# Optimization experiments

Hardware: AMD Instinct MI355X
Metric: run time of the kernel (lower is better)

The kernel has to match this reference:

```python
import jax, jax.numpy as jnp
import numpy as np

EMBED_DIM = 1024
HEAD_NUM = 16
NEG = 100000.0


def setup_inputs() -> dict:
    key = jax.random.key(0)
    k1, k2, k3, k4, k5 = jax.random.split(key, 5)
    B, S, E = 2, 2048, EMBED_DIM
    return {
        "x": jax.random.normal(k1, (B, S, E), dtype=jnp.float32),
        "w_attn": jax.random.normal(k2, (E, 3 * E), dtype=jnp.float32) * 0.02,
        "b_attn": jax.random.normal(k3, (3 * E,), dtype=jnp.float32) * 0.02,
        "w_proj": jax.random.normal(k4, (E, E), dtype=jnp.float32) * 0.02,
        "b_proj": jax.random.normal(k5, (E,), dtype=jnp.float32) * 0.02,
    }


def reference(x, w_attn, b_attn, w_proj, b_proj):
    B, S, E = x.shape
    H = HEAD_NUM
    d = E // H
    dk = jnp.asarray(d, x.dtype) ** 0.5  # (embed_dim // head_num) ** 0.5

    qkv = x @ w_attn + b_attn                      # [B, S, 3E]
    qkv = qkv.reshape(B, S, H, 3 * d)              # split heads BEFORE chunk (as in source)
    qkv = jnp.swapaxes(qkv, 1, 2)                  # [B, H, S, 3d]
    q, k, v = jnp.split(qkv, 3, axis=-1)           # each [B, H, S, d]

    w = jnp.einsum("bhqd,bhkd->bhqk", q, k) / dk   # [B, H, S, S]
    mask = jnp.tril(jnp.ones((S, S), dtype=x.dtype))
    w = w * mask - (1.0 - mask) * NEG              # exact masking math of source
    w = jax.nn.softmax(w, axis=-1)                 # dropout omitted (eval mode)

    a = jnp.einsum("bhqk,bhkd->bhqd", w, v)        # [B, H, S, d]
    a = jnp.swapaxes(a, 1, 2).reshape(B, S, E)     # [B, S, E]
    h = a @ w_proj + b_proj                        # resi dropout omitted (eval mode)
    return h
```

## Files before the change

### kernel.cpp

```cpp
#include <hip/hip_runtime.h>
#include <hip/hip_bf16.h>

#define BB 2
#define SS 2048
#define EE 1024
#define HH 16
#define DD 64
#define MM (BB*SS)
#define N1 (3*EE)

typedef __attribute__((ext_vector_type(4))) float f32x4;
typedef __attribute__((ext_vector_type(16))) float f32x16;
typedef __attribute__((ext_vector_type(8))) short bf16x8;
typedef __attribute__((ext_vector_type(4))) unsigned int u32x4;
typedef __attribute__((ext_vector_type(2))) unsigned int u32x2;

__device__ __forceinline__ ushort f2bf(float f){
  union { float f; unsigned u; } v; v.f = f;
  unsigned r = v.u + 0x7fffu + ((v.u >> 16) & 1u);
  return (ushort)(r >> 16);
}

__device__ __forceinline__ float bf2f(ushort u){
  union { unsigned u; float f; } v; v.u = ((unsigned)u) << 16; return v.f;
}

__device__ __forceinline__ unsigned cvt_pk(float a, float b){
  unsigned r; asm("v_cvt_pk_bf16_f32 %0, %1, %2" : "=v"(r) : "v"(a), "v"(b)); return r;
}

__device__ __forceinline__ float exp2_fast(float x){
  float r; asm("v_exp_f32 %0, %1" : "=v"(r) : "v"(x)); return r;
}

__device__ __forceinline__ u32x2 pl32swap(unsigned a, unsigned b){
  return __builtin_amdgcn_permlane32_swap(a, b, false, false);
}

__device__ __forceinline__ void gload16(const void* g, void* l){
  __builtin_amdgcn_global_load_lds(
      (const __attribute__((address_space(1))) unsigned*)g,
      (__attribute__((address_space(3))) unsigned*)l, 16, 0, 0);
}

__global__ __launch_bounds__(256) void prep_kernel(const float* __restrict__ x, ushort* __restrict__ xb,
    const float* __restrict__ wa, ushort* __restrict__ waT,
    const float* __restrict__ wp, ushort* __restrict__ wpT){
  __shared__ float t[32][33];
  const int bid = blockIdx.x, tid = threadIdx.x;
  if (bid < 4096){
    int i = bid*256 + tid;
    const float4 f = reinterpret_cast<const float4*>(x)[i];
    ushort4 o; o.x=f2bf(f.x); o.y=f2bf(f.y); o.z=f2bf(f.z); o.w=f2bf(f.w);
    reinterpret_cast<ushort4*>(xb)[i] = o;
  } else {
    const float* in; ushort* out; int N, nx, b;
    if (bid < 7168){ b = bid - 4096; in = wa; out = waT; N = N1; nx = N1/32; }
    else           { b = bid - 7168; in = wp; out = wpT; N = EE; nx = EE/32; }
    const int n0 = (b % nx)*32, k0 = (b / nx)*32;
    const int tx = tid & 31, ty = tid >> 5;
    for (int r = ty; r < 32; r += 8)
      t[r][tx] = in[(size_t)(k0+r)*N + n0 + tx];
    __syncthreads();
    for (int r = ty; r < 32; r += 8)
      out[(size_t)(n0+r)*EE + k0 + tx] = f2bf(t[tx][r]);
  }
}

__global__ __launch_bounds__(512) void gemm_qkv(const ushort* __restrict__ A,
    const ushort* __restrict__ Bt, const float* __restrict__ bias,
    ushort* __restrict__ q_, ushort* __restrict__ k_, ushort* __restrict__ v_,
    int M, int N, int K){
  __shared__ ushort As[256*64];
  __shared__ ushort Bs[128*64];
  const int tid = threadIdx.x;
  const int lane = tid & 63, w = tid >> 6;
  const int nx = gridDim.x;
  const int nwg = nx * gridDim.y;
  const int flat = blockIdx.y*nx + blockIdx.x;
  const int sw = (flat & 7)*(nwg >> 3) + (flat >> 3);
  const int m0 = (sw / nx)*256, n0 = (sw % nx)*128;
  const int wm = (w >> 1)*64, wn = (w & 1)*64;
  const int lr = lane & 15, g4 = lane >> 4;
  const int csr = lane >> 3;
  const int gcb = ((lane & 7) ^ csr)*8;
  const int sw7 = lr & 7;

  f32x4 acc[4][4] = {};
  for (int k0 = 0; k0 < K; k0 += 64){
    #pragma unroll
    for (int i = 0; i < 4; ++i){
      const int c = w*4 + i;
      gload16(A + (size_t)(m0 + c*8 + csr)*K + k0 + gcb, &As[(c*8)*64]);
    }
    #pragma unroll
    for (int i = 0; i < 2; ++i){
      const int c = w*2 + i;
      gload16(Bt + (size_t)(n0 + c*8 + csr)*K + k0 + gcb, &Bs[(c*8)*64]);
    }
    __syncthreads();
    #pragma unroll
    for (int kk = 0; kk < 2; ++kk){
      bf16x8 af[4], bfr[4];
      #pragma unroll
      for (int m = 0; m < 4; ++m)
        af[m] = *reinterpret_cast<bf16x8*>(&As[(wm + m*16 + lr)*64 + (((kk*4 + g4) ^ sw7)*8)]);
      #pragma unroll
      for (int n = 0; n < 4; ++n)
        bfr[n] = *reinterpret_cast<bf16x8*>(&Bs[(wn + n*16 + lr)*64 + (((kk*4 + g4) ^ sw7)*8)]);
      __builtin_amdgcn_s_setprio(1);
      #pragma unroll
      for (int m = 0; m < 4; ++m)
        #pragma unroll
        for (int n = 0; n < 4; ++n)
          acc[m][n] = __builtin_amdgcn_mfma_f32_16x16x32_bf16(af[m], bfr[n], acc[m][n], 0, 0, 0);
      __builtin_amdgcn_s_setprio(0);
    }
    __syncthreads();
  }
  #pragma unroll
  for (int m = 0; m < 4; ++m){
    #pragma unroll
    for (int n = 0; n < 4; ++n){
      int col = n0 + wn + n*16 + lr;
      float bv = bias[col];
      #pragma unroll
      for (int r = 0; r < 4; ++r){
        int row = m0 + wm + m*16 + (lane >> 4)*4 + r;
        float v = acc[m][n][r] + bv;
        int b = row >> 11, s = row & 2047;
        int h = col / 192, t = col - h*192;
        ushort u = f2bf(v);
        size_t bh = (size_t)(b*HH + h);
        if (t < 64)       q_[(bh*SS + s)*DD + t]        = u;
        else if (t < 128) k_[(bh*SS + s)*DD + (t-64)]   = u;
        else              v_[(bh*DD + (t-128))*SS + s]  = u;
      }
    }
  }
}

__global__ __launch_bounds__(256) void gemm_proj(const ushort* __restrict__ A,
    const ushort* __restrict__ Bt, const float* __restrict__ bias,
    float* __restrict__ of, int M, int N, int K){
  __shared__ ushort As[128*64];
  __shared__ ushort Bs[128*64];
  const int tid = threadIdx.x;
  const int lane = tid & 63, w = tid >> 6;
  const int nx = gridDim.x;
  const int nwg = nx * gridDim.y;
  const int flat = blockIdx.y*nx + blockIdx.x;
  const int sw = (flat & 7)*(nwg >> 3) + (flat >> 3);
  const int m0 = (sw / nx)*128, n0 = (sw % nx)*128;
  const int wm = (w >> 1)*64, wn = (w & 1)*64;
  const int lr = lane & 15, g4 = lane >> 4;
  const int c0 = w*4;
  const int csr = lane >> 3;
  const int gcb = ((lane & 7) ^ csr)*8;
  const int sw7 = lr & 7;

  f32x4 acc[4][4] = {};
  for (int k0 = 0; k0 < K; k0 += 64){
    #pragma unroll
    for (int i = 0; i < 4; ++i){
      const int c = c0 + i;
      gload16(A  + (size_t)(m0 + c*8 + csr)*K + k0 + gcb, &As[(c*8)*64]);
      gload16(Bt + (size_t)(n0 + c*8 + csr)*K + k0 + gcb, &Bs[(c*8)*64]);
    }
    __syncthreads();
    #pragma unroll
    for (int kk = 0; kk < 2; ++kk){
      bf16x8 af[4], bfr[4];
      #pragma unroll
      for (int m = 0; m < 4; ++m)
        af[m] = *reinterpret_cast<bf16x8*>(&As[(wm + m*16 + lr)*64 + (((kk*4 + g4) ^ sw7)*8)]);
      #pragma unroll
      for (int n = 0; n < 4; ++n)
        bfr[n] = *reinterpret_cast<bf16x8*>(&Bs[(wn + n*16 + lr)*64 + (((kk*4 + g4) ^ sw7)*8)]);
      __builtin_amdgcn_s_setprio(1);
      #pragma unroll
      for (int m = 0; m < 4; ++m)
        #pragma unroll
        for (int n = 0; n < 4; ++n)
          acc[m][n] = __builtin_amdgcn_mfma_f32_16x16x32_bf16(af[m], bfr[n], acc[m][n], 0, 0, 0);
      __builtin_amdgcn_s_setprio(0);
    }
    __syncthreads();
  }
  #pragma unroll
  for (int m = 0; m < 4; ++m){
    #pragma unroll
    for (int n = 0; n < 4; ++n){
      int col = n0 + wn + n*16 + lr;
      float bv = bias[col];
      #pragma unroll
      for (int r = 0; r < 4; ++r){
        int row = m0 + wm + m*16 + (lane >> 4)*4 + r;
        of[(size_t)row*N + col] = acc[m][n][r] + bv;
      }
    }
  }
}

#define SCL 0.18033688f
__global__ __launch_bounds__(256,3) void attn2(const ushort* __restrict__ Qg,
    const ushort* __restrict__ Kg, const ushort* __restrict__ Vg,
    ushort* __restrict__ aout, ushort* __restrict__ pbuf,
    float* __restrict__ s0b, float* __restrict__ s1b){
  __shared__ __align__(16) ushort Kl[3][64*64];
  __shared__ __align__(16) ushort Vl[3][64*64];
  const int tid = threadIdx.x, lane = tid & 63, wv = tid >> 6;
  const int bh = blockIdx.x;
  const int c  = blockIdx.y;
  int qt, t0, t1, half;
  if (c < 8){ qt = c; t0 = 0; t1 = 2*(c+1); half = -1; }
  else { int i = c - 8; qt = 8 + (i >> 1); int n = qt + 1; half = i & 1;
         t0 = half ? n : 0; t1 = half ? 2*n : n; }
  const int b = bh >> 4, h = bh & 15;
  const int q0 = qt*128;
  const int ql = lane & 31, g = lane >> 5;
  const int qrow = q0 + wv*32 + ql;
  const int qminw = q0 + wv*32;
  const int qmaxw = qminw + 31;

  const ushort* Qp = Qg + ((size_t)bh*SS + qrow)*DD;
  bf16x8 qf[4];
  #pragma unroll
  for (int s = 0; s < 4; ++s)
    qf[s] = *(const bf16x8*)(Qp + s*16 + g*8);

  f32x16 ot[2] = {};
  float sr = 0.f;

  const int csr = lane >> 3;
  const int gcb = ((lane & 7) ^ csr)*8;
  const ushort* Kbase = Kg + (size_t)bh*SS*DD;
  const ushort* Vbase = Vg + (size_t)bh*DD*SS;
  const int nv = (qmaxw >> 6) + 1;
  const int swq = (ql & 7);

  auto stage = [&](int t, int bi){
    const int k0 = t*64;
    #pragma unroll
    for (int i = 0; i < 2; ++i){
      const int ch = wv*2 + i;
      gload16(Kbase + (size_t)(k0 + ch*8 + csr)*DD + gcb, &Kl[bi][(ch*8)*64]);
      gload16(Vbase + (size_t)(ch*8 + csr)*SS + k0 + gcb, &Vl[bi][(ch*8)*64]);
    }
  };

  auto qk = [&](int t, int bi, f32x16& s0, f32x16& s1){
    const ushort* Kc = &Kl[bi][0];
    f32x16 a0 = {}, a1 = {};
    __builtin_amdgcn_s_setprio(1);
    #pragma unroll
    for (int s = 0; s < 4; ++s){
      bf16x8 kf0 = *(const bf16x8*)&Kc[ ql     *64 + (((2*s + g) ^ swq)*8)];
      bf16x8 kf1 = *(const bf16x8*)&Kc[(32+ql) *64 + (((2*s + g) ^ swq)*8)];
      a0 = __builtin_amdgcn_mfma_f32_32x32x16_bf16(kf0, qf[s], a0, 0, 0, 0);
      a1 = __builtin_amdgcn_mfma_f32_32x32x16_bf16(kf1, qf[s], a1, 0, 0, 0);
    }
    __builtin_amdgcn_s_setprio(0);
    const int k0 = t*64;
    if (k0 + 63 > qminw){
      #pragma unroll
      for (int r = 0; r < 16; ++r){
        int kg0 = k0 + (r & 3) + 8*(r >> 2) + 4*g;
        a0[r] = (kg0 > qrow) ? -1e30f : a0[r];
        a1[r] = (kg0 + 32 > qrow) ? -1e30f : a1[r];
      }
    }
    s0 = a0; s1 = a1;
  };

  auto smpv = [&](int bi, f32x16& s0, f32x16& s1){
    float p[2][16];
    #pragma unroll
    for (int r = 0; r < 16; ++r){
      p[0][r] = exp2_fast(s0[r]*SCL);
      p[1][r] = exp2_fast(s1[r]*SCL);
    }
    float s8[8];
    #pragma unroll
    for (int i = 0; i < 8; ++i)
      s8[i] = (p[0][i] + p[0][i+8]) + (p[1][i] + p[1][i+8]);
    float ts = ((s8[0]+s8[1]) + (s8[2]+s8[3])) + ((s8[4]+s8[5]) + (s8[6]+s8[7]));
    { u32x2 rs = pl32swap(__float_as_uint(ts), __float_as_uint(ts));
      ts = __uint_as_float(rs[0]) + __uint_as_float(rs[1]); }
    sr += ts;

    const ushort* Vc = &Vl[bi][0];
    __builtin_amdgcn_s_setprio(1);
    #pragma unroll
    for (int kf = 0; kf < 2; ++kf){
      #pragma unroll
      for (int s2 = 0; s2 < 2; ++s2){
        const int base = s2*8;
        unsigned u0 = cvt_pk(p[kf][base+0], p[kf][base+1]);
        unsigned u1 = cvt_pk(p[kf][base+2], p[kf][base+3]);
        unsigned u2 = cvt_pk(p[kf][base+4], p[kf][base+5]);
        unsigned u3 = cvt_pk(p[kf][base+6], p[kf][base+7]);
        u32x2 r0 = pl32swap(u0, u2);
        u32x2 r1 = pl32swap(u1, u3);
        union { u32x4 u; bf16x8 hv; } pw;
        pw.u[0] = r0[0]; pw.u[1] = r1[0]; pw.u[2] = r0[1]; pw.u[3] = r1[1];
        const int cbv = 4*kf + 2*s2 + g;
        bf16x8 v0f = *(const bf16x8*)&Vc[ ql     *64 + ((cbv ^ swq)*8)];
        bf16x8 v1f = *(const bf16x8*)&Vc[(32+ql) *64 + ((cbv ^ swq)*8)];
        ot[0] = __builtin_amdgcn_mfma_f32_32x32x16_bf16(v0f, pw.hv, ot[0], 0, 0, 0);
        ot[1] = __builtin_amdgcn_mfma_f32_32x32x16_bf16(v1f, pw.hv, ot[1], 0, 0, 0);
      }
    }
    __builtin_amdgcn_s_setprio(0);
  };

  stage(t0, 0);
  stage(t0 + 1, 1);
  int bi = 0;
  for (int t = t0; t < t1; ++t){
    if (t + 1 < t1) { asm volatile("s_waitcnt vmcnt(4)" ::: "memory"); }
    else            { asm volatile("s_waitcnt vmcnt(0)" ::: "memory"); }
    __builtin_amdgcn_s_barrier();
    __builtin_amdgcn_sched_barrier(0);
    if (t + 2 < t1){
      int bs = bi + 2; if (bs >= 3) bs -= 3;
      stage(t + 2, bs);
    }
    if (t < nv){
      f32x16 s0, s1;
      qk(t, bi, s0, s1);
      smpv(bi, s0, s1);
    }
    ++bi; if (bi == 3) bi = 0;
  }

  const float inv = 1.f / sr;
  if (half == 1){
    const int pr = ((qt - 8)*32 + bh)*128 + wv*32 + ql;
    #pragma unroll
    for (int df = 0; df < 2; ++df){
      #pragma unroll
      for (int t = 0; t < 4; ++t){
        ushort4 o4;
        o4.x = f2bf(ot[df][t*4+0]*inv);
        o4.y = f2bf(ot[df][t*4+1]*inv);
        o4.z = f2bf(ot[df][t*4+2]*inv);
        o4.w = f2bf(ot[df][t*4+3]*inv);
        int d = df*32 + 8*t + 4*g;
        *(ushort4*)&pbuf[(size_t)pr*64 + d] = o4;
      }
    }
    if (g == 0) s1b[pr] = sr;
  } else {
    const size_t obase = ((size_t)b*SS + qrow)*EE + h*DD;
    #pragma unroll
    for (int df = 0; df < 2; ++df){
      #pragma unroll
      for (int t = 0; t < 4; ++t){
        ushort4 o4;
        o4.x = f2bf(ot[df][t*4+0]*inv);
        o4.y = f2bf(ot[df][t*4+1]*inv);
        o4.z = f2bf(ot[df][t*4+2]*inv);
        o4.w = f2bf(ot[df][t*4+3]*inv);
        int d = df*32 + 8*t + 4*g;
        *(ushort4*)&aout[obase + d] = o4;
      }
    }
    if (half == 0){
      const int pr = ((qt - 8)*32 + bh)*128 + wv*32 + ql;
      if (g == 0) s0b[pr] = sr;
    }
  }
}

__global__ __launch_bounds__(256) void combine_kernel(ushort* __restrict__ ab,
    const ushort* __restrict__ pbuf, const float* __restrict__ s0b,
    const float* __restrict__ s1b){
  const int idx = blockIdx.x*256 + threadIdx.x;
  const int d4 = (idx & 15)*4;
  const int rr = (idx >> 4) & 127;
  const int pb = idx >> 11;
  const int qt8 = pb >> 5, bh = pb & 31;
  const int b = bh >> 4, h = bh & 15;
  const int pr = pb*128 + rr;
  const float s0 = s0b[pr], s1 = s1b[pr];
  const float wn = 1.f/(s0 + s1);
  const float w0 = s0*wn, w1 = s1*wn;
  const size_t ao = ((size_t)(b*SS + (8 + qt8)*128 + rr))*EE + h*DD + d4;
  const size_t po = (size_t)pr*64 + d4;
  ushort4 a = *(const ushort4*)&ab[ao];
  ushort4 p = *(const ushort4*)&pbuf[po];
  ushort4 o;
  o.x = f2bf(w0*bf2f(a.x) + w1*bf2f(p.x));
  o.y = f2bf(w0*bf2f(a.y) + w1*bf2f(p.y));
  o.z = f2bf(w0*bf2f(a.z) + w1*bf2f(p.z));
  o.w = f2bf(w0*bf2f(a.w) + w1*bf2f(p.w));
  *(ushort4*)&ab[ao] = o;
}

extern "C" void kernel_launch(void* const* d_in, const int* in_sizes, int n_in,
                              void* d_out, int out_size, void* d_ws, size_t ws_size,
                              hipStream_t stream){
  const float* x      = (const float*)d_in[0];
  const float* w_attn = (const float*)d_in[1];
  const float* b_attn = (const float*)d_in[2];
  const float* w_proj = (const float*)d_in[3];
  const float* b_proj = (const float*)d_in[4];
  float* out = (float*)d_out;

  ushort* ws   = (ushort*)d_ws;
  ushort* xb   = ws;
  ushort* waT  = xb  + (size_t)MM*EE;
  ushort* wpT  = waT + (size_t)N1*EE;
  ushort* qb_  = wpT + (size_t)EE*EE;
  ushort* kb_  = qb_ + (size_t)MM*EE;
  ushort* vTb  = kb_ + (size_t)MM*EE;
  ushort* ab   = vTb + (size_t)MM*EE;
  ushort* pbuf = xb;
  float*  s0b  = (float*)waT;
  float*  s1b  = s0b + 8*32*128;

  prep_kernel<<<8192, 256, 0, stream>>>(x, xb, w_attn, waT, w_proj, wpT);
  gemm_qkv<<<dim3(N1/128, MM/256), 512, 0, stream>>>(xb, waT, b_attn, qb_, kb_, vTb, MM, N1, EE);
  attn2<<<dim3(BB*HH, 24), 256, 0, stream>>>(qb_, kb_, vTb, ab, pbuf, s0b, s1b);
  combine_kernel<<<2048, 256, 0, stream>>>(ab, pbuf, s0b, s1b);
  gemm_proj<<<dim3(EE/128, MM/128), 256, 0, stream>>>(ab, wpT, b_proj, out, MM, EE, EE);
}
```

Baseline: 114.2 us.

## Split causal attention into up to four key-range parts and shrink GEMM tiles

The attention kernel now splits each query tile's key range into 1 to 4 parts depending on tile depth, launching 40 blocks per head instead of 24. Partial outputs and row sums go to a generalized buffer that the combine kernel merges. The K/V staging drops from triple to double buffering and occupancy is raised to 5 blocks per CU. Both GEMMs use smaller tiles to get more workgroups: 128x128 with 256 threads for QKV and 64x128 for the projection. The aim is better load balance and CU fill, at the cost of more combine traffic and less latency hiding in the attention loop.

```diff
diff --git a/kernel.cpp b/kernel.cpp
--- a/kernel.cpp
+++ b/kernel.cpp
@@ -42,6 +42,8 @@
       (const __attribute__((address_space(1))) unsigned*)g,
       (__attribute__((address_space(3))) unsigned*)l, 16, 0, 0);
 }
+
+__device__ __constant__ int exoff_c[16] = {0,0,0,0, 0,1,2,3, 4,6,8,10, 12,15,18,21};
 
 __global__ __launch_bounds__(256) void prep_kernel(const float* __restrict__ x, ushort* __restrict__ xb,
     const float* __restrict__ wa, ushort* __restrict__ waT,
@@ -67,82 +69,10 @@
   }
 }
 
-__global__ __launch_bounds__(512) void gemm_qkv(const ushort* __restrict__ A,
+__global__ __launch_bounds__(256) void gemm_qkv(const ushort* __restrict__ A,
     const ushort* __restrict__ Bt, const float* __restrict__ bias,
     ushort* __restrict__ q_, ushort* __restrict__ k_, ushort* __restrict__ v_,
     int M, int N, int K){
-  __shared__ ushort As[256*64];
-  __shared__ ushort Bs[128*64];
-  const int tid = threadIdx.x;
-  const int lane = tid & 63, w = tid >> 6;
-  const int nx = gridDim.x;
-  const int nwg = nx * gridDim.y;
-  const int flat = blockIdx.y*nx + blockIdx.x;
-  const int sw = (flat & 7)*(nwg >> 3) + (flat >> 3);
-  const int m0 = (sw / nx)*256, n0 = (sw % nx)*128;
-  const int wm = (w >> 1)*64, wn = (w & 1)*64;
-  const int lr = lane & 15, g4 = lane >> 4;
-  const int csr = lane >> 3;
-  const int gcb = ((lane & 7) ^ csr)*8;
-  const int sw7 = lr & 7;
-
-  f32x4 acc[4][4] = {};
-  for (int k0 = 0; k0 < K; k0 += 64){
-    #pragma unroll
-    for (int i = 0; i < 4; ++i){
-      const int c = w*4 + i;
-      gload16(A + (size_t)(m0 + c*8 + csr)*K + k0 + gcb, &As[(c*8)*64]);
-    }
-    #pragma unroll
-    for (int i = 0; i < 2; ++i){
-      const int c = w*2 + i;
-      gload16(Bt + (size_t)(n0 + c*8 + csr)*K + k0 + gcb, &Bs[(c*8)*64]);
-    }
-    __syncthreads();
-    #pragma unroll
-    for (int kk = 0; kk < 2; ++kk){
-      bf16x8 af[4], bfr[4];
-      #pragma unroll
-      for (int m = 0; m < 4; ++m)
-        af[m] = *reinterpret_cast<bf16x8*>(&As[(wm + m*16 + lr)*64 + (((kk*4 + g4) ^ sw7)*8)]);
-      #pragma unroll
-      for (int n = 0; n < 4; ++n)
-        bfr[n] = *reinterpret_cast<bf16x8*>(&Bs[(wn + n*16 + lr)*64 + (((kk*4 + g4) ^ sw7)*8)]);
-      __builtin_amdgcn_s_setprio(1);
-      #pragma unroll
-      for (int m = 0; m < 4; ++m)
-        #pragma unroll
-        for (int n = 0; n < 4; ++n)
-          acc[m][n] = __builtin_amdgcn_mfma_f32_16x16x32_bf16(af[m], bfr[n], acc[m][n], 0, 0, 0);
-      __builtin_amdgcn_s_setprio(0);
-    }
-    __syncthreads();
-  }
-  #pragma unroll
-  for (int m = 0; m < 4; ++m){
-    #pragma unroll
-    for (int n = 0; n < 4; ++n){
-      int col = n0 + wn + n*16 + lr;
-      float bv = bias[col];
-      #pragma unroll
-      for (int r = 0; r < 4; ++r){
-        int row = m0 + wm + m*16 + (lane >> 4)*4 + r;
-        float v = acc[m][n][r] + bv;
-        int b = row >> 11, s = row & 2047;
-        int h = col / 192, t = col - h*192;
-        ushort u = f2bf(v);
-        size_t bh = (size_t)(b*HH + h);
-        if (t < 64)       q_[(bh*SS + s)*DD + t]        = u;
-        else if (t < 128) k_[(bh*SS + s)*DD + (t-64)]   = u;
-        else              v_[(bh*DD + (t-128))*SS + s]  = u;
-      }
-    }
-  }
-}
-
-__global__ __launch_bounds__(256) void gemm_proj(const ushort* __restrict__ A,
-    const ushort* __restrict__ Bt, const float* __restrict__ bias,
-    float* __restrict__ of, int M, int N, int K){
   __shared__ ushort As[128*64];
   __shared__ ushort Bs[128*64];
   const int tid = threadIdx.x;
@@ -196,6 +126,77 @@
       #pragma unroll
       for (int r = 0; r < 4; ++r){
         int row = m0 + wm + m*16 + (lane >> 4)*4 + r;
+        float v = acc[m][n][r] + bv;
+        int b = row >> 11, s = row & 2047;
+        int h = col / 192, t = col - h*192;
+        ushort u = f2bf(v);
+        size_t bh = (size_t)(b*HH + h);
+        if (t < 64)       q_[(bh*SS + s)*DD + t]        = u;
+        else if (t < 128) k_[(bh*SS + s)*DD + (t-64)]   = u;
+        else              v_[(bh*DD + (t-128))*SS + s]  = u;
+      }
+    }
+  }
+}
+
+__global__ __launch_bounds__(256) void gemm_proj(const ushort* __restrict__ A,
+    const ushort* __restrict__ Bt, const float* __restrict__ bias,
+    float* __restrict__ of, int M, int N, int K){
+  __shared__ ushort As[64*64];
+  __shared__ ushort Bs[128*64];
+  const int tid = threadIdx.x;
+  const int lane = tid & 63, w = tid >> 6;
+  const int nx = gridDim.x;
+  const int nwg = nx * gridDim.y;
+  const int flat = blockIdx.y*nx + blockIdx.x;
+  const int sw = (flat & 7)*(nwg >> 3) + (flat >> 3);
+  const int m0 = (sw / nx)*64, n0 = (sw % nx)*128;
+  const int lr = lane & 15, g4 = lane >> 4;
+  const int csr = lane >> 3;
+  const int gcb = ((lane & 7) ^ csr)*8;
+  const int sw7 = lr & 7;
+
+  f32x4 acc[4][2] = {};
+  for (int k0 = 0; k0 < K; k0 += 64){
+    #pragma unroll
+    for (int i = 0; i < 2; ++i){
+      const int c = w*2 + i;
+      gload16(A + (size_t)(m0 + c*8 + csr)*K + k0 + gcb, &As[(c*8)*64]);
+    }
+    #pragma unroll
+    for (int i = 0; i < 4; ++i){
+      const int c = w*4 + i;
+      gload16(Bt + (size_t)(n0 + c*8 + csr)*K + k0 + gcb, &Bs[(c*8)*64]);
+    }
+    __syncthreads();
+    #pragma unroll
+    for (int kk = 0; kk < 2; ++kk){
+      bf16x8 af[4], bfr[2];
+      #pragma unroll
+      for (int m = 0; m < 4; ++m)
+        af[m] = *reinterpret_cast<bf16x8*>(&As[(m*16 + lr)*64 + (((kk*4 + g4) ^ sw7)*8)]);
+      #pragma unroll
+      for (int n = 0; n < 2; ++n)
+        bfr[n] = *reinterpret_cast<bf16x8*>(&Bs[(w*32 + n*16 + lr)*64 + (((kk*4 + g4) ^ sw7)*8)]);
+      __builtin_amdgcn_s_setprio(1);
+      #pragma unroll
+      for (int m = 0; m < 4; ++m)
+        #pragma unroll
+        for (int n = 0; n < 2; ++n)
+          acc[m][n] = __builtin_amdgcn_mfma_f32_16x16x32_bf16(af[m], bfr[n], acc[m][n], 0, 0, 0);
+      __builtin_amdgcn_s_setprio(0);
+    }
+    __syncthreads();
+  }
+  #pragma unroll
+  for (int m = 0; m < 4; ++m){
+    #pragma unroll
+    for (int n = 0; n < 2; ++n){
+      int col = n0 + w*32 + n*16 + lr;
+      float bv = bias[col];
+      #pragma unroll
+      for (int r = 0; r < 4; ++r){
+        int row = m0 + m*16 + g4*4 + r;
         of[(size_t)row*N + col] = acc[m][n][r] + bv;
       }
     }
@@ -203,19 +204,24 @@
 }
 
 #define SCL 0.18033688f
-__global__ __launch_bounds__(256,3) void attn2(const ushort* __restrict__ Qg,
+__global__ __launch_bounds__(256,5) void attn2(const ushort* __restrict__ Qg,
     const ushort* __restrict__ Kg, const ushort* __restrict__ Vg,
     ushort* __restrict__ aout, ushort* __restrict__ pbuf,
-    float* __restrict__ s0b, float* __restrict__ s1b){
-  __shared__ __align__(16) ushort Kl[3][64*64];
-  __shared__ __align__(16) ushort Vl[3][64*64];
+    float* __restrict__ sb){
+  __shared__ __align__(16) ushort Kl[2][64*64];
+  __shared__ __align__(16) ushort Vl[2][64*64];
   const int tid = threadIdx.x, lane = tid & 63, wv = tid >> 6;
   const int bh = blockIdx.x;
   const int c  = blockIdx.y;
-  int qt, t0, t1, half;
-  if (c < 8){ qt = c; t0 = 0; t1 = 2*(c+1); half = -1; }
-  else { int i = c - 8; qt = 8 + (i >> 1); int n = qt + 1; half = i & 1;
-         t0 = half ? n : 0; t1 = half ? 2*n : n; }
+  int qt, part;
+  if (c < 4)       { qt = c;                 part = 0; }
+  else if (c < 12) { qt = 4 + ((c-4) >> 1);  part = (c-4) & 1; }
+  else if (c < 24) { qt = 8 + (c-12)/3;      part = (c-12)%3; }
+  else             { qt = 12 + ((c-24) >> 2); part = (c-24) & 3; }
+  const int T = 2*(qt+1), np = (qt >> 2) + 1;
+  const int base = T/np, rem = T%np;
+  const int t0 = part*base + (part < rem ? part : rem);
+  const int t1 = t0 + base + (part < rem ? 1 : 0);
   const int b = bh >> 4, h = bh & 15;
   const int q0 = qt*128;
   const int ql = lane & 31, g = lane >> 5;
@@ -295,11 +301,11 @@
     for (int kf = 0; kf < 2; ++kf){
       #pragma unroll
       for (int s2 = 0; s2 < 2; ++s2){
-        const int base = s2*8;
-        unsigned u0 = cvt_pk(p[kf][base+0], p[kf][base+1]);
-        unsigned u1 = cvt_pk(p[kf][base+2], p[kf][base+3]);
-        unsigned u2 = cvt_pk(p[kf][base+4], p[kf][base+5]);
-        unsigned u3 = cvt_pk(p[kf][base+6], p[kf][base+7]);
+        const int bse = s2*8;
+        unsigned u0 = cvt_pk(p[kf][bse+0], p[kf][bse+1]);
+        unsigned u1 = cvt_pk(p[kf][bse+2], p[kf][bse+3]);
+        unsigned u2 = cvt_pk(p[kf][bse+4], p[kf][bse+5]);
+        unsigned u3 = cvt_pk(p[kf][bse+6], p[kf][bse+7]);
         u32x2 r0 = pl32swap(u0, u2);
         u32x2 r1 = pl32swap(u1, u3);
         union { u32x4 u; bf16x8 hv; } pw;
@@ -315,43 +321,24 @@
   };
 
   stage(t0, 0);
-  stage(t0 + 1, 1);
   int bi = 0;
   for (int t = t0; t < t1; ++t){
-    if (t + 1 < t1) { asm volatile("s_waitcnt vmcnt(4)" ::: "memory"); }
-    else            { asm volatile("s_waitcnt vmcnt(0)" ::: "memory"); }
+    asm volatile("s_waitcnt vmcnt(0)" ::: "memory");
     __builtin_amdgcn_s_barrier();
     __builtin_amdgcn_sched_barrier(0);
-    if (t + 2 < t1){
-      int bs = bi + 2; if (bs >= 3) bs -= 3;
-      stage(t + 2, bs);
-    }
+    if (t + 1 < t1) stage(t + 1, bi ^ 1);
     if (t < nv){
       f32x16 s0, s1;
       qk(t, bi, s0, s1);
       smpv(bi, s0, s1);
     }
-    ++bi; if (bi == 3) bi = 0;
+    bi ^= 1;
   }
 
   const float inv = 1.f / sr;
-  if (half == 1){
-    const int pr = ((qt - 8)*32 + bh)*128 + wv*32 + ql;
-    #pragma unroll
-    for (int df = 0; df < 2; ++df){
-      #pragma unroll
-      for (int t = 0; t < 4; ++t){
-        ushort4 o4;
-        o4.x = f2bf(ot[df][t*4+0]*inv);
-        o4.y = f2bf(ot[df][t*4+1]*inv);
-        o4.z = f2bf(ot[df][t*4+2]*inv);
-        o4.w = f2bf(ot[df][t*4+3]*inv);
-        int d = df*32 + 8*t + 4*g;
-        *(ushort4*)&pbuf[(size_t)pr*64 + d] = o4;
-      }
-    }
-    if (g == 0) s1b[pr] = sr;
-  } else {
+  const int prow = wv*32 + ql;
+  if (g == 0) sb[(size_t)((qt*4 + part)*32 + bh)*128 + prow] = sr;
+  if (part == 0){
     const size_t obase = ((size_t)b*SS + qrow)*EE + h*DD;
     #pragma unroll
     for (int df = 0; df < 2; ++df){
@@ -366,35 +353,61 @@
         *(ushort4*)&aout[obase + d] = o4;
       }
     }
-    if (half == 0){
-      const int pr = ((qt - 8)*32 + bh)*128 + wv*32 + ql;
-      if (g == 0) s0b[pr] = sr;
+  } else {
+    const int e = exoff_c[qt] + part - 1;
+    const size_t pbase = ((size_t)(e*32 + bh)*128 + prow)*64;
+    #pragma unroll
+    for (int df = 0; df < 2; ++df){
+      #pragma unroll
+      for (int t = 0; t < 4; ++t){
+        ushort4 o4;
+        o4.x = f2bf(ot[df][t*4+0]*inv);
+        o4.y = f2bf(ot[df][t*4+1]*inv);
+        o4.z = f2bf(ot[df][t*4+2]*inv);
+        o4.w = f2bf(ot[df][t*4+3]*inv);
+        int d = df*32 + 8*t + 4*g;
+        *(ushort4*)&pbuf[pbase + d] = o4;
+      }
     }
   }
 }
 
 __global__ __launch_bounds__(256) void combine_kernel(ushort* __restrict__ ab,
-    const ushort* __restrict__ pbuf, const float* __restrict__ s0b,
-    const float* __restrict__ s1b){
+    const ushort* __restrict__ pbuf, const float* __restrict__ sb){
   const int idx = blockIdx.x*256 + threadIdx.x;
   const int d4 = (idx & 15)*4;
   const int rr = (idx >> 4) & 127;
-  const int pb = idx >> 11;
-  const int qt8 = pb >> 5, bh = pb & 31;
+  const int z  = idx >> 11;
+  const int qt = 4 + (z >> 5), bh = z & 31;
   const int b = bh >> 4, h = bh & 15;
-  const int pr = pb*128 + rr;
-  const float s0 = s0b[pr], s1 = s1b[pr];
-  const float wn = 1.f/(s0 + s1);
-  const float w0 = s0*wn, w1 = s1*wn;
-  const size_t ao = ((size_t)(b*SS + (8 + qt8)*128 + rr))*EE + h*DD + d4;
-  const size_t po = (size_t)pr*64 + d4;
+  const int np = (qt >> 2) + 1;
+  float s[4] = {0.f, 0.f, 0.f, 0.f};
+  float stot = 0.f;
+  #pragma unroll
+  for (int p = 0; p < 4; ++p){
+    if (p < np){
+      s[p] = sb[(size_t)((qt*4 + p)*32 + bh)*128 + rr];
+      stot += s[p];
+    }
+  }
+  const float wn = 1.f / stot;
+  const size_t ao = ((size_t)(b*SS + qt*128 + rr))*EE + h*DD + d4;
   ushort4 a = *(const ushort4*)&ab[ao];
-  ushort4 p = *(const ushort4*)&pbuf[po];
+  float ax = s[0]*wn*bf2f(a.x), ay = s[0]*wn*bf2f(a.y);
+  float az = s[0]*wn*bf2f(a.z), aw = s[0]*wn*bf2f(a.w);
+  #pragma unroll
+  for (int p = 1; p < 4; ++p){
+    if (p < np){
+      const int e = exoff_c[qt] + p - 1;
+      const size_t po = ((size_t)(e*32 + bh)*128 + rr)*64 + d4;
+      ushort4 q = *(const ushort4*)&pbuf[po];
+      const float wp_ = s[p]*wn;
+      ax += wp_*bf2f(q.x); ay += wp_*bf2f(q.y);
+      az += wp_*bf2f(q.z); aw += wp_*bf2f(q.w);
+    }
+  }
   ushort4 o;
-  o.x = f2bf(w0*bf2f(a.x) + w1*bf2f(p.x));
-  o.y = f2bf(w0*bf2f(a.y) + w1*bf2f(p.y));
-  o.z = f2bf(w0*bf2f(a.z) + w1*bf2f(p.z));
-  o.w = f2bf(w0*bf2f(a.w) + w1*bf2f(p.w));
+  o.x = f2bf(ax); o.y = f2bf(ay); o.z = f2bf(az); o.w = f2bf(aw);
   *(ushort4*)&ab[ao] = o;
 }
 
@@ -417,12 +430,11 @@
   ushort* vTb  = kb_ + (size_t)MM*EE;
   ushort* ab   = vTb + (size_t)MM*EE;
   ushort* pbuf = xb;
-  float*  s0b  = (float*)waT;
-  float*  s1b  = s0b + 8*32*128;
+  float*  sbuf = (float*)(pbuf + (size_t)24*32*128*64);
 
   prep_kernel<<<8192, 256, 0, stream>>>(x, xb, w_attn, waT, w_proj, wpT);
-  gemm_qkv<<<dim3(N1/128, MM/256), 512, 0, stream>>>(xb, waT, b_attn, qb_, kb_, vTb, MM, N1, EE);
-  attn2<<<dim3(BB*HH, 24), 256, 0, stream>>>(qb_, kb_, vTb, ab, pbuf, s0b, s1b);
-  combine_kernel<<<2048, 256, 0, stream>>>(ab, pbuf, s0b, s1b);
-  gemm_proj<<<dim3(EE/128, MM/128), 256, 0, stream>>>(ab, wpT, b_proj, out, MM, EE, EE);
-}
+  gemm_qkv<<<dim3(N1/128, MM/128), 256, 0, stream>>>(xb, waT, b_attn, qb_, kb_, vTb, MM, N1, EE);
+  attn2<<<dim3(BB*HH, 40), 256, 0, stream>>>(qb_, kb_, vTb, ab, pbuf, sbuf);
+  combine_kernel<<<3072, 256, 0, stream>>>(ab, pbuf, sbuf);
+  gemm_proj<<<dim3(EE/128, MM/64), 256, 0, stream>>>(ab, wpT, b_proj, out, MM, EE, EE);
+}
```

Measured after the change: 128.4 us. 12.5% more time.
